# Kernel optimization log

Measured on AMD Instinct MI355X. Metric: run time of the kernel, lower is better.

## Reference

```python
import jax, jax.numpy as jnp
import numpy as np

H = 256
SLOTS = 64
EPS = 1e-5


def setup_inputs() -> dict:
    key = jax.random.key(0)
    ks = jax.random.split(key, 10)
    B, T = 4096, 128
    # original feeds integer-valued floats in [0,10)
    x = jax.random.randint(ks[0], (B, T, 1), 0, 10).astype(jnp.float32)
    s = 0.02
    return {
        "x": x,
        "W_embed": jax.random.normal(ks[1], (1, H), jnp.float32) * s,
        "b_embed": jnp.zeros((H,), jnp.float32),
        "W_update": jax.random.normal(ks[2], (H, H), jnp.float32) * s,
        "b_update": jnp.zeros((H,), jnp.float32),
        "gamma": jnp.ones((H,), jnp.float32),
        "beta": jnp.zeros((H,), jnp.float32),
        "W_out": jax.random.normal(ks[3], (H, 10), jnp.float32) * s,
        "b_out": jnp.zeros((10,), jnp.float32),
        "context_strength": jnp.asarray(0.2, jnp.float32),
    }


def _layernorm(h, gamma, beta):
    mu = jnp.mean(h, axis=-1, keepdims=True)
    var = jnp.mean(jnp.square(h - mu), axis=-1, keepdims=True)
    return (h - mu) * jax.lax.rsqrt(var + EPS) * gamma + beta


def reference(x, W_embed, b_embed, W_update, b_update, gamma, beta, W_out, b_out, context_strength):
    B, T, _ = x.shape
    cs = jax.nn.sigmoid(context_strength)
    h0 = jnp.zeros((B, H), x.dtype)
    mem0 = jnp.zeros((B, SLOTS, H), x.dtype)
    ptrs = jnp.arange(T, dtype=jnp.int32) % SLOTS  # pointer is identical across batch
    xs = (jnp.transpose(x, (1, 0, 2)), ptrs)        # [T,B,1], [T]

    def step(carry, inputs):
        h, mem = carry
        xt, ptr = inputs
        inp = jnp.tanh(xt @ W_embed + b_embed)          # [B,H]
        context = jax.lax.dynamic_slice_in_dim(mem, ptr, 1, axis=1)[:, 0, :]  # gather slot
        combined = inp + cs * context
        h = jnp.tanh((combined + h) @ W_update + b_update)
        h = _layernorm(h, gamma, beta)
        mem = jax.lax.dynamic_update_slice_in_dim(mem, h[:, None, :], ptr, axis=1)
        return (h, mem), None

    (h, _), _ = jax.lax.scan(step, (h0, mem0), xs)
    return h @ W_out + b_out
```

## Files before the change

kernel.cpp:

```cpp
#include <hip/hip_runtime.h>
#include <hip/hip_bf16.h>
#include <hip/hip_fp16.h>
#include <stdint.h>

#define H 256
#define BT 4096
#define TS 128
#define ROWS 16
#define NBLK 256
#define NTH 1024
#define LD 260
#define LDP 264

typedef __attribute__((ext_vector_type(8))) _Float16 f16x8;
typedef __attribute__((ext_vector_type(4))) float f32x4;

__device__ __forceinline__ float exp2_fast(float x){ float r; asm("v_exp_f32 %0, %1" : "=v"(r) : "v"(x)); return r; }
__device__ __forceinline__ float rcp_fast(float x){ float r; asm("v_rcp_f32 %0, %1" : "=v"(r) : "v"(x)); return r; }
__device__ __forceinline__ float rsq_fast(float x){ float r; asm("v_rsq_f32 %0, %1" : "=v"(r) : "v"(x)); return r; }
__device__ __forceinline__ float tanh_fast(float x){
  float e = exp2_fast(x * 2.8853900817779268f);
  return 1.0f - 2.0f * rcp_fast(e + 1.0f);
}
__device__ __forceinline__ unsigned pk_f16(float a, float b){
  __half2 h2 = __float22half2_rn(make_float2(a, b));
  union { __half2 h; unsigned u; } cv; cv.h = h2; return cv.u;
}
__device__ __forceinline__ float f16_lo(unsigned v){
  float r; asm("v_cvt_f32_f16 %0, %1" : "=v"(r) : "v"(v)); return r;
}
__device__ __forceinline__ unsigned pk_bf16(float a, float b){
  __hip_bfloat162 h2 = __float22bfloat162_rn(make_float2(a, b));
  union { __hip_bfloat162 h; unsigned u; } cv; cv.h = h2; return cv.u;
}
__device__ __forceinline__ void bar_lgkm(){ asm volatile("s_waitcnt lgkmcnt(0)\n\ts_barrier" ::: "memory"); }

template<int CTRL>
__device__ __forceinline__ float dpp_add(float x){
  int y = __builtin_amdgcn_update_dpp(0, __float_as_int(x), CTRL, 0xf, 0xf, false);
  return x + __int_as_float(y);
}
#define ROR1 0x121
#define ROR2 0x122
#define ROR4 0x124
#define ROR8 0x128
#define BC15 0x142
#define BC31 0x143
__device__ __forceinline__ float lane_f(float v, int n){
  return __int_as_float(__builtin_amdgcn_readlane(__float_as_int(v), n));
}

__global__ __launch_bounds__(NTH, 4) void wp_kernel(
    const float* __restrict__ x, const float* __restrict__ We, const float* __restrict__ be,
    const float* __restrict__ Wu, const float* __restrict__ bu, const float* __restrict__ gm,
    const float* __restrict__ bt, const float* __restrict__ Wo, const float* __restrict__ bo,
    const float* __restrict__ cst, unsigned short* __restrict__ hist, float* __restrict__ out,
    int use_hist)
{
  __shared__ __align__(16) float emb[10][LD];
  __shared__ __align__(16) unsigned hp[8][LDP];
  __shared__ __align__(16) float hfin[ROWS][LDP];
  __shared__ __align__(16) unsigned short afrag[8][64][8];

  const int tid = threadIdx.x;
  const int r0 = blockIdx.x * ROWS;
  const int w  = tid >> 6;
  const int l  = tid & 63;
  const int fr = l & 15;
  const int fo = l >> 4;
  const int c0 = 16*w + fr;
  const int rp = w >> 1;
  const int sh = (w & 1) << 4;

  float cs;
  { float c = cst[0]; cs = rcp_fast(1.0f + exp2_fast(-c * 1.4426950408889634f)); }

  unsigned xw = 0;
  if (l < 32) {
    const float* xp = x + (size_t)(r0 + w)*TS + 4*l;
    unsigned b0 = (unsigned)(int)(xp[0] + 0.5f);
    unsigned b1 = (unsigned)(int)(xp[1] + 0.5f);
    unsigned b2 = (unsigned)(int)(xp[2] + 0.5f);
    unsigned b3 = (unsigned)(int)(xp[3] + 0.5f);
    xw = b0 | (b1 << 8) | (b2 << 16) | (b3 << 24);
  }

  for (int i = tid; i < 10*H; i += NTH) {
    int v = i >> 8, k = i & 255;
    emb[v][k] = tanh_fast((float)v * We[k] + be[k]);
  }

  f16x8 wf[8];
  #pragma unroll
  for (int kc = 0; kc < 8; ++kc) {
    #pragma unroll
    for (int i = 0; i < 8; ++i) {
      int kg = 32*kc + 8*fo + i;
      wf[kc][i] = (_Float16)Wu[(size_t)kg*H + c0];
    }
  }
  const float bval = bu[c0];
  f32x4 g4 = *(const f32x4*)(gm + 4*l);
  f32x4 b4 = *(const f32x4*)(bt + 4*l);

  const int XR = l ^ (2*fo);
  const unsigned short* const abase = &afrag[0][0][0];
  int ao[8];
  #pragma unroll
  for (int kc = 0; kc < 8; ++kc) ao[kc] = kc*512 + (XR ^ kc)*8;
  const int wkc = l >> 3, wfo = (l >> 1) & 3, we = l & 1;
  unsigned short* const aw = &afrag[wkc][(w + 16*wfo) ^ wkc ^ (2*wfo)][4*we];
  const unsigned* const hpr = &hp[rp][4*l];
  const size_t histLane = (size_t)(r0 + w)*H + 4*l;
  __syncthreads();

  {
    int xv = __builtin_amdgcn_readlane(xw, 0) & 0xff;
    f32x4 e4 = *(const f32x4*)&emb[xv][4*l];
    uint2 p = { pk_f16(e4[0], e4[1]), pk_f16(e4[2], e4[3]) };
    *(uint2*)aw = p;
  }
  __syncthreads();

  uint2 cP = {0,0}, cQ = {0,0};

#define PHASE2() do { \
    f32x4 acc = {bval, bval, bval, bval}; \
    _Pragma("unroll") \
    for (int kc = 0; kc < 8; ++kc) { \
      f16x8 af = *(const f16x8*)(abase + ao[kc]); \
      acc = __builtin_amdgcn_mfma_f32_16x16x32_f16(af, wf[kc], acc, 0, 0, 0); \
    } \
    hp[2*fo  ][c0] = pk_f16(tanh_fast(acc[0]), tanh_fast(acc[1])); \
    hp[2*fo+1][c0] = pk_f16(tanh_fast(acc[2]), tanh_fast(acc[3])); \
  } while(0)

#define LN_STATS_HV() \
    uint4 qv = *(const uint4*)hpr; \
    float h0 = f16_lo(qv.x >> sh); \
    float h1 = f16_lo(qv.y >> sh); \
    float h2 = f16_lo(qv.z >> sh); \
    float h3 = f16_lo(qv.w >> sh); \
    float s1 = (h0+h1) + (h2+h3); \
    float s2 = h0*h0; \
    s2 = fmaf(h1,h1,s2); s2 = fmaf(h2,h2,s2); s2 = fmaf(h3,h3,s2); \
    s1 = dpp_add<ROR1>(s1); s1 = dpp_add<ROR2>(s1); s1 = dpp_add<ROR4>(s1); s1 = dpp_add<ROR8>(s1); \
    s2 = dpp_add<ROR1>(s2); s2 = dpp_add<ROR2>(s2); s2 = dpp_add<ROR4>(s2); s2 = dpp_add<ROR8>(s2); \
    s1 = dpp_add<BC15>(s1); s1 = dpp_add<BC31>(s1); \
    s2 = dpp_add<BC15>(s2); s2 = dpp_add<BC31>(s2); \
    float S1 = lane_f(s1, 63); \
    float S2 = lane_f(s2, 63); \
    float mu  = S1 * 0.00390625f; \
    float var = S2 * 0.00390625f - mu*mu; \
    float rs  = rsq_fast(var + 1e-5f); \
    float hv0 = fmaf(h0-mu, rs*g4[0], b4[0]); \
    float hv1 = fmaf(h1-mu, rs*g4[1], b4[1]); \
    float hv2 = fmaf(h2-mu, rs*g4[2], b4[2]); \
    float hv3 = fmaf(h3-mu, rs*g4[3], b4[3]);

#define PHASE3(HW, CUSE, CLOAD, tt) do { \
    unsigned xwv = (unsigned)__builtin_amdgcn_readlane(xw, ((tt)+1) >> 2); \
    int xv = (xwv >> (8*(((tt)+1) & 3))) & 0xff; \
    f32x4 e4 = *(const f32x4*)&emb[xv][4*l]; \
    LN_STATS_HV(); \
    float a0, a1, a2, a3; \
    if ((CUSE) && use_hist) { \
      a0 = fmaf(cs, __uint_as_float(cP.x << 16),         e4[0] + hv0); \
      a1 = fmaf(cs, __uint_as_float(cP.x & 0xffff0000u), e4[1] + hv1); \
      a2 = fmaf(cs, __uint_as_float(cP.y << 16),         e4[2] + hv2); \
      a3 = fmaf(cs, __uint_as_float(cP.y & 0xffff0000u), e4[3] + hv3); \
    } else { \
      a0 = e4[0] + hv0; a1 = e4[1] + hv1; a2 = e4[2] + hv2; a3 = e4[3] + hv3; \
    } \
    uint2 pkk = { pk_f16(a0,a1), pk_f16(a2,a3) }; \
    *(uint2*)aw = pkk; \
    if ((HW) && use_hist) { \
      uint2 hb = { pk_bf16(hv0,hv1), pk_bf16(hv2,hv3) }; \
      *(uint2*)(hist + (size_t)(tt)*(BT*H) + histLane) = hb; \
    } \
    if ((CUSE) || (CLOAD)) { cP = cQ; } \
    if ((CLOAD) && use_hist) \
      cQ = *(const uint2*)(hist + (size_t)((tt)-61)*(BT*H) + histLane); \
  } while(0)

  for (int t = 0; t < 61; ++t)  { PHASE2(); bar_lgkm(); PHASE3(1,0,0,t); bar_lgkm(); }
  for (int t = 61; t < 63; ++t) { PHASE2(); bar_lgkm(); PHASE3(1,0,1,t); bar_lgkm(); }
  {                               PHASE2(); bar_lgkm(); PHASE3(1,1,1,63); bar_lgkm(); }
  for (int t = 64; t < 125; ++t){ PHASE2(); bar_lgkm(); PHASE3(0,1,1,t); bar_lgkm(); }
  for (int t = 125; t < 127; ++t){PHASE2(); bar_lgkm(); PHASE3(0,1,0,t); bar_lgkm(); }
  {
    PHASE2(); bar_lgkm();
    LN_STATS_HV();
    f32x4 o = {hv0, hv1, hv2, hv3};
    *(f32x4*)&hfin[w][4*l] = o;
  }

  __syncthreads();
  if (tid < ROWS * 10) {
    int r = tid / 10, c = tid % 10;
    float acc = bo[c];
    for (int k = 0; k < H; ++k) acc += hfin[r][k] * Wo[k*10 + c];
    out[((size_t)(r0 + r))*10 + c] = acc;
  }
}

extern "C" void kernel_launch(void* const* d_in, const int* in_sizes, int n_in,
                              void* d_out, int out_size, void* d_ws, size_t ws_size,
                              hipStream_t stream) {
  const float* x   = (const float*)d_in[0];
  const float* We  = (const float*)d_in[1];
  const float* be  = (const float*)d_in[2];
  const float* Wu  = (const float*)d_in[3];
  const float* bu  = (const float*)d_in[4];
  const float* gm  = (const float*)d_in[5];
  const float* bt  = (const float*)d_in[6];
  const float* Wo  = (const float*)d_in[7];
  const float* bo  = (const float*)d_in[8];
  const float* cst = (const float*)d_in[9];
  float* out = (float*)d_out;

  size_t need = (size_t)64 * BT * H * sizeof(unsigned short);
  int use_hist = (ws_size >= need) ? 1 : 0;

  hipLaunchKernelGGL(wp_kernel, dim3(NBLK), dim3(NTH), 0, stream,
                     x, We, be, Wu, bu, gm, bt, Wo, bo, cst,
                     (unsigned short*)d_ws, out, use_hist);
}
```

Before: 146.6 us.

## Halve rows per block and give each wave two MFMA column tiles

Blocks now handle 8 batch rows with 512 threads instead of 16 rows with 1024, and launch twice as many blocks. Each wave computes two 16-column tiles with independent MFMA accumulators, which adds instruction-level parallelism in the recurrent matmul. Half of the MFMA output rows (the padding rows) are masked off on store, so the matrix units do redundant work. Register pressure roughly doubles for the weight fragments, which could limit occupancy.

```diff
diff --git a/kernel.cpp b/kernel.cpp
--- a/kernel.cpp
+++ b/kernel.cpp
@@ -6,9 +6,9 @@
 #define H 256
 #define BT 4096
 #define TS 128
-#define ROWS 16
-#define NBLK 256
-#define NTH 1024
+#define ROWS 8
+#define NBLK 512
+#define NTH 512
 #define LD 260
 #define LDP 264
 
@@ -58,7 +58,7 @@
     int use_hist)
 {
   __shared__ __align__(16) float emb[10][LD];
-  __shared__ __align__(16) unsigned hp[8][LDP];
+  __shared__ __align__(16) unsigned hp[4][LDP];
   __shared__ __align__(16) float hfin[ROWS][LDP];
   __shared__ __align__(16) unsigned short afrag[8][64][8];
 
@@ -68,7 +68,7 @@
   const int l  = tid & 63;
   const int fr = l & 15;
   const int fo = l >> 4;
-  const int c0 = 16*w + fr;
+  const int c0 = 32*w + fr, c1 = c0 + 16;
   const int rp = w >> 1;
   const int sh = (w & 1) << 4;
 
@@ -78,11 +78,8 @@
   unsigned xw = 0;
   if (l < 32) {
     const float* xp = x + (size_t)(r0 + w)*TS + 4*l;
-    unsigned b0 = (unsigned)(int)(xp[0] + 0.5f);
-    unsigned b1 = (unsigned)(int)(xp[1] + 0.5f);
-    unsigned b2 = (unsigned)(int)(xp[2] + 0.5f);
-    unsigned b3 = (unsigned)(int)(xp[3] + 0.5f);
-    xw = b0 | (b1 << 8) | (b2 << 16) | (b3 << 24);
+    xw = ((unsigned)(int)(xp[0]+0.5f)) | ((unsigned)(int)(xp[1]+0.5f) << 8)
+       | ((unsigned)(int)(xp[2]+0.5f) << 16) | ((unsigned)(int)(xp[3]+0.5f) << 24);
   }
 
   for (int i = tid; i < 10*H; i += NTH) {
@@ -90,20 +87,21 @@
     emb[v][k] = tanh_fast((float)v * We[k] + be[k]);
   }
 
-  f16x8 wf[8];
+  f16x8 wf0[8], wf1[8];
   #pragma unroll
   for (int kc = 0; kc < 8; ++kc) {
     #pragma unroll
     for (int i = 0; i < 8; ++i) {
       int kg = 32*kc + 8*fo + i;
-      wf[kc][i] = (_Float16)Wu[(size_t)kg*H + c0];
+      wf0[kc][i] = (_Float16)Wu[(size_t)kg*H + c0];
+      wf1[kc][i] = (_Float16)Wu[(size_t)kg*H + c1];
     }
   }
-  const float bval = bu[c0];
+  const float bval0 = bu[c0], bval1 = bu[c1];
   f32x4 g4 = *(const f32x4*)(gm + 4*l);
   f32x4 b4 = *(const f32x4*)(bt + 4*l);
 
-  const int XR = l ^ (2*fo);
+  const int XR = (l & 55) ^ (2*fo);
   const unsigned short* const abase = &afrag[0][0][0];
   int ao[8];
   #pragma unroll
@@ -125,14 +123,20 @@
   uint2 cP = {0,0}, cQ = {0,0};
 
 #define PHASE2() do { \
-    f32x4 acc = {bval, bval, bval, bval}; \
+    f32x4 acc0 = {bval0, bval0, bval0, bval0}; \
+    f32x4 acc1 = {bval1, bval1, bval1, bval1}; \
     _Pragma("unroll") \
     for (int kc = 0; kc < 8; ++kc) { \
       f16x8 af = *(const f16x8*)(abase + ao[kc]); \
-      acc = __builtin_amdgcn_mfma_f32_16x16x32_f16(af, wf[kc], acc, 0, 0, 0); \
-    } \
-    hp[2*fo  ][c0] = pk_f16(tanh_fast(acc[0]), tanh_fast(acc[1])); \
-    hp[2*fo+1][c0] = pk_f16(tanh_fast(acc[2]), tanh_fast(acc[3])); \
+      acc0 = __builtin_amdgcn_mfma_f32_16x16x32_f16(af, wf0[kc], acc0, 0, 0, 0); \
+      acc1 = __builtin_amdgcn_mfma_f32_16x16x32_f16(af, wf1[kc], acc1, 0, 0, 0); \
+    } \
+    if (fo < 2) { \
+      hp[2*fo  ][c0] = pk_f16(tanh_fast(acc0[0]), tanh_fast(acc0[1])); \
+      hp[2*fo+1][c0] = pk_f16(tanh_fast(acc0[2]), tanh_fast(acc0[3])); \
+      hp[2*fo  ][c1] = pk_f16(tanh_fast(acc1[0]), tanh_fast(acc1[1])); \
+      hp[2*fo+1][c1] = pk_f16(tanh_fast(acc1[2]), tanh_fast(acc1[3])); \
+    } \
   } while(0)
 
 #define LN_STATS_HV() \
```

After: 195.9 us. +33.7%, slower.
